# Optimization experiments

Hardware: AMD Instinct MI355X
Metric: run time of the kernel (lower is better)

## Reference

```python
import jax, jax.numpy as jnp
import numpy as np

L = 6
LN_EPS = 1e-5

def _ln(x):
    # LayerNorm over last dim, no affine (matches nn.LayerNorm(D, elementwise_affine=False))
    m = jnp.mean(x, axis=-1, keepdims=True)
    v = jnp.var(x, axis=-1, keepdims=True)
    return (x - m) / jnp.sqrt(v + LN_EPS)

def setup_inputs() -> dict:
    key = jax.random.key(0)
    ks = jax.random.split(key, 6)
    B, S, N, D, V = 2, 2048, 4096, 1024, 32000
    return {
        "input_": jax.random.randint(ks[0], (B, S), 0, V),
        "emb": jax.random.normal(ks[1], (V, D), jnp.float32) * 0.02,
        "Dx": jax.random.normal(ks[2], (D, N), jnp.float32) * 0.02,
        "Dy": jax.random.normal(ks[3], (D, N), jnp.float32) * 0.02,
        "E": jax.random.normal(ks[4], (N, D), jnp.float32) * 0.02,
        "readout": jax.random.normal(ks[5], (D, V), jnp.float32) * 0.02,
    }

def reference(input_, emb, Dx, Dy, E, readout):
    v_ast = emb[input_]  # [B,S,D]
    for _ in range(L):
        x = jax.nn.relu(jnp.einsum('bsd,dn->bsn', v_ast, Dx))  # [B,S,N]
        # linear attention Q@K.mT@V reassociated: x @ (x.mT @ v)
        kv = jnp.einsum('bsn,bsd->bnd', x, v_ast)              # [B,N,D]
        a_ast = jnp.einsum('bsn,bnd->bsd', x, kv)              # [B,S,D]
        y = jax.nn.relu(jnp.einsum('bsd,dn->bsn', a_ast, Dy)) * x  # [B,S,N]
        v_ast = _ln(v_ast + _ln(jnp.einsum('bsn,nd->bsd', y, E)))
    return jnp.einsum('bsd,dv->bsv', v_ast, readout)  # [B,S,vocab]
```

## Files before the change

kernel.cpp:

```cpp
#include <hip/hip_runtime.h>
#include <stdint.h>

typedef unsigned short u16;
typedef __bf16 bf16x8 __attribute__((ext_vector_type(8)));
typedef float  floatx4 __attribute__((ext_vector_type(4)));
typedef u16    ushort4v __attribute__((ext_vector_type(4)));
typedef u16    ushort8v __attribute__((ext_vector_type(8)));

#define B_ 2
#define S_ 2048
#define D_ 1024
#define N_ 4096
#define V_ 32000
#define R_ (B_ * S_)
#define L_ 6

__device__ __forceinline__ u16 f2bf(float f) {
  union { float f; uint32_t u; } v; v.f = f;
  uint32_t r = v.u + 0x7fffu + ((v.u >> 16) & 1u);
  return (u16)(r >> 16);
}
__device__ __forceinline__ float bf2f(u16 h) {
  union { uint32_t u; float f; } v; v.u = ((uint32_t)h) << 16;
  return v.f;
}

__device__ __forceinline__ void gload16(const u16* g, u16* l) {
  auto* gp = (__attribute__((address_space(1))) void*)const_cast<u16*>(g);
  auto* lp = (__attribute__((address_space(3))) void*)l;
  __builtin_amdgcn_global_load_lds(gp, lp, 16, 0, 0);
}

template<int MODE>
__global__ __launch_bounds__(256)
void gemm_bt(const u16* __restrict__ A, const u16* __restrict__ BT,
             void* __restrict__ Cv, const u16* __restrict__ Mul,
             int M, int N, int K, size_t sA, size_t sBT, size_t sC)
{
  __shared__ __align__(16) u16 As[128 * 32];
  __shared__ __align__(16) u16 Bs[128 * 32];

  const int tid  = threadIdx.x;
  const int lane = tid & 63;
  const int wave = tid >> 6;
  const int r = lane & 15;
  const int q = lane >> 4;
  const int wm = (wave >> 1) << 6;
  const int wn = (wave & 1) << 6;

  const int nby = gridDim.y;
  const int bid = blockIdx.y * gridDim.x + blockIdx.x;
  const int bx  = bid / nby;
  const int by  = bid - bx * nby;
  const long m0 = (long)by * 128;
  const long n0 = (long)bx * 128;

  const u16* Ab = A  + (size_t)blockIdx.z * sA;
  const u16* Bb = BT + (size_t)blockIdx.z * sBT;

  const int srow = tid >> 2;
  const int scol = (tid & 3) << 3;
  const u16* a_src0 = Ab + (size_t)(m0 + srow) * K + scol;
  const u16* a_src1 = a_src0 + (size_t)64 * K;
  const u16* b_src0 = Bb + (size_t)(n0 + srow) * K + scol;
  const u16* b_src1 = b_src0 + (size_t)64 * K;
  u16* a_d0 = &As[wave * 512];
  u16* a_d1 = &As[2048 + wave * 512];
  u16* b_d0 = &Bs[wave * 512];
  u16* b_d1 = &Bs[2048 + wave * 512];

  const floatx4 zero = {0.f, 0.f, 0.f, 0.f};
  floatx4 acc[4][4];
#pragma unroll
  for (int i = 0; i < 4; ++i)
#pragma unroll
    for (int j = 0; j < 4; ++j) acc[i][j] = zero;

  for (int kt = 0; kt < K; kt += 32) {
    __syncthreads();
    gload16(a_src0 + kt, a_d0);
    gload16(a_src1 + kt, a_d1);
    gload16(b_src0 + kt, b_d0);
    gload16(b_src1 + kt, b_d1);
    __syncthreads();

    bf16x8 af[4], bfr[4];
#pragma unroll
    for (int i = 0; i < 4; ++i)
      af[i]  = *(const bf16x8*)&As[(wm + i*16 + r) * 32 + (q << 3)];
#pragma unroll
    for (int j = 0; j < 4; ++j)
      bfr[j] = *(const bf16x8*)&Bs[(wn + j*16 + r) * 32 + (q << 3)];
#pragma unroll
    for (int i = 0; i < 4; ++i)
#pragma unroll
      for (int j = 0; j < 4; ++j)
        acc[i][j] = __builtin_amdgcn_mfma_f32_16x16x32_bf16(af[i], bfr[j], acc[i][j], 0, 0, 0);
  }

  const long crow0 = m0 + wm + (q << 2);
  const long ccol0 = n0 + wn + r;
#pragma unroll
  for (int i = 0; i < 4; ++i) {
#pragma unroll
    for (int j = 0; j < 4; ++j) {
      const long col = ccol0 + j * 16;
#pragma unroll
      for (int ii = 0; ii < 4; ++ii) {
        const long row = crow0 + i * 16 + ii;
        float v = acc[i][j][ii];
        if (MODE == 1 || MODE == 2) v = fmaxf(v, 0.f);
        const size_t off = (size_t)row * N + col;
        if (MODE == 2) v *= bf2f(Mul[off]);
        if (MODE == 3) (((float*)Cv) + (size_t)blockIdx.z * sC)[off] = v;
        else           (((u16*)Cv)   + (size_t)blockIdx.z * sC)[off] = f2bf(v);
      }
    }
  }
}

__global__ __launch_bounds__(256)
void transpose_bf16(const u16* __restrict__ src, u16* __restrict__ dst, int R, int C)
{
  __shared__ __align__(16) u16 tile[64][68];
  const int t = threadIdx.x;
  const long r0 = (long)blockIdx.y * 64;
  const long c0 = (long)blockIdx.x * 64;
  const int tc = (t & 15) << 2;
  const int tr = t >> 4;
#pragma unroll
  for (int i = 0; i < 4; ++i) {
    const int rr = tr + (i << 4);
    *(ushort4v*)&tile[rr][tc] = *(const ushort4v*)(src + (size_t)(r0 + rr) * C + c0 + tc);
  }
  __syncthreads();
#pragma unroll
  for (int i = 0; i < 4; ++i) {
    const int cc = tr + (i << 4);
    ushort4v v;
#pragma unroll
    for (int j = 0; j < 4; ++j) v[j] = tile[tc + j][cc];
    *(ushort4v*)(dst + (size_t)(c0 + cc) * R + r0 + tc) = v;
  }
}

__global__ __launch_bounds__(256)
void cvt_transpose(const float* __restrict__ src, u16* __restrict__ dst, int R, int C)
{
  __shared__ __align__(16) u16 tile[64][68];
  const int t = threadIdx.x;
  const long r0 = (long)blockIdx.y * 64;
  const long c0 = (long)blockIdx.x * 64;
  const int tc = (t & 15) << 2;
  const int tr = t >> 4;
#pragma unroll
  for (int i = 0; i < 4; ++i) {
    const int rr = tr + (i << 4);
    const float4 v = *(const float4*)(src + (size_t)(r0 + rr) * C + c0 + tc);
    ushort4v h = {f2bf(v.x), f2bf(v.y), f2bf(v.z), f2bf(v.w)};
    *(ushort4v*)&tile[rr][tc] = h;
  }
  __syncthreads();
#pragma unroll
  for (int i = 0; i < 4; ++i) {
    const int cc = tr + (i << 4);
    ushort4v v;
#pragma unroll
    for (int j = 0; j < 4; ++j) v[j] = tile[tc + j][cc];
    *(ushort4v*)(dst + (size_t)(c0 + cc) * R + r0 + tc) = v;
  }
}

__global__ __launch_bounds__(256)
void embed_k(const int* __restrict__ idx, const float* __restrict__ emb,
             float* __restrict__ vf, u16* __restrict__ vb)
{
  const size_t row = blockIdx.x;
  const int t = threadIdx.x;
  const int id = idx[row];
  const float4 x = ((const float4*)(emb + (size_t)id * D_))[t];
  ((float4*)(vf + row * D_))[t] = x;
  ushort4v h = {f2bf(x.x), f2bf(x.y), f2bf(x.z), f2bf(x.w)};
  ((ushort4v*)(vb + row * D_))[t] = h;
}

__device__ __forceinline__ float block_sum(float v, float* red, int t) {
#pragma unroll
  for (int o = 32; o > 0; o >>= 1) v += __shfl_down(v, o, 64);
  __syncthreads();
  if ((t & 63) == 0) red[t >> 6] = v;
  __syncthreads();
  return red[0] + red[1] + red[2] + red[3];
}

__global__ __launch_bounds__(256)
void ln_k(const float* __restrict__ z, float* __restrict__ vf, u16* __restrict__ vb)
{
  __shared__ float red[4];
  const int t = threadIdx.x;
  const size_t row = blockIdx.x;
  const float4 zv = ((const float4*)(z + row * D_))[t];
  float s = zv.x + zv.y + zv.z + zv.w;
  const float mean = block_sum(s, red, t) * (1.0f / D_);
  float4 d;
  d.x = zv.x - mean; d.y = zv.y - mean; d.z = zv.z - mean; d.w = zv.w - mean;
  float s2 = d.x*d.x + d.y*d.y + d.z*d.z + d.w*d.w;
  const float var = block_sum(s2, red, t) * (1.0f / D_);
  const float inv = rsqrtf(var + 1e-5f);
  const float4 vv = ((const float4*)(vf + row * D_))[t];
  float4 w;
  w.x = vv.x + d.x * inv; w.y = vv.y + d.y * inv;
  w.z = vv.z + d.z * inv; w.w = vv.w + d.w * inv;
  float sw = w.x + w.y + w.z + w.w;
  const float mean2 = block_sum(sw, red, t) * (1.0f / D_);
  float4 d2;
  d2.x = w.x - mean2; d2.y = w.y - mean2; d2.z = w.z - mean2; d2.w = w.w - mean2;
  float s22 = d2.x*d2.x + d2.y*d2.y + d2.z*d2.z + d2.w*d2.w;
  const float var2 = block_sum(s22, red, t) * (1.0f / D_);
  const float inv2 = rsqrtf(var2 + 1e-5f);
  float4 o;
  o.x = d2.x * inv2; o.y = d2.y * inv2; o.z = d2.z * inv2; o.w = d2.w * inv2;
  ((float4*)(vf + row * D_))[t] = o;
  ushort4v h = {f2bf(o.x), f2bf(o.y), f2bf(o.z), f2bf(o.w)};
  ((ushort4v*)(vb + row * D_))[t] = h;
}

extern "C" void kernel_launch(void* const* d_in, const int* in_sizes, int n_in,
                              void* d_out, int out_size, void* d_ws, size_t ws_size,
                              hipStream_t stream)
{
  const int*   inp = (const int*)d_in[0];
  const float* emb = (const float*)d_in[1];
  const float* Dx  = (const float*)d_in[2];
  const float* Dy  = (const float*)d_in[3];
  const float* E   = (const float*)d_in[4];
  const float* ro  = (const float*)d_in[5];
  float* out = (float*)d_out;

  char* p = (char*)d_ws;
  auto take = [&](size_t n) { char* q = p; p += (n + 255) & ~(size_t)255; return q; };
  float* vf  = (float*)take((size_t)R_ * D_ * 4);
  float* zf  = (float*)take((size_t)R_ * D_ * 4);
  u16* vb    = (u16*)take((size_t)R_ * D_ * 2);
  u16* vbT   = (u16*)take((size_t)R_ * D_ * 2);
  u16* xb    = (u16*)take((size_t)R_ * N_ * 2);
  u16* xbT   = (u16*)take((size_t)R_ * N_ * 2);
  u16* yb    = (u16*)take((size_t)R_ * N_ * 2);
  u16* kvT   = (u16*)take((size_t)B_ * D_ * N_ * 2);
  u16* ab    = (u16*)take((size_t)R_ * D_ * 2);
  u16* DxT   = (u16*)take((size_t)D_ * N_ * 2);
  u16* DyT   = (u16*)take((size_t)D_ * N_ * 2);
  u16* ET    = (u16*)take((size_t)D_ * N_ * 2);
  u16* roT   = (u16*)take((size_t)D_ * V_ * 2);

  const dim3 blk(256);

  cvt_transpose<<<dim3(N_/64, D_/64), blk, 0, stream>>>(Dx, DxT, D_, N_);
  cvt_transpose<<<dim3(N_/64, D_/64), blk, 0, stream>>>(Dy, DyT, D_, N_);
  cvt_transpose<<<dim3(D_/64, N_/64), blk, 0, stream>>>(E,  ET,  N_, D_);
  cvt_transpose<<<dim3(V_/64, D_/64), blk, 0, stream>>>(ro, roT, D_, V_);

  embed_k<<<dim3(R_), blk, 0, stream>>>(inp, emb, vf, vb);
  for (int b = 0; b < B_; ++b)
    transpose_bf16<<<dim3(D_/64, S_/64), blk, 0, stream>>>(
        vb + (size_t)b*S_*D_, vbT + (size_t)b*D_*S_, S_, D_);

  for (int l = 0; l < L_; ++l) {
    gemm_bt<1><<<dim3(N_/128, R_/128, 1), blk, 0, stream>>>(
        vb, DxT, xb, nullptr, R_, N_, D_, 0, 0, 0);
    for (int b = 0; b < B_; ++b)
      transpose_bf16<<<dim3(N_/64, S_/64), blk, 0, stream>>>(
          xb + (size_t)b*S_*N_, xbT + (size_t)b*N_*S_, S_, N_);
    gemm_bt<0><<<dim3(N_/128, D_/128, B_), blk, 0, stream>>>(
        vbT, xbT, kvT, nullptr, D_, N_, S_,
        (size_t)D_*S_, (size_t)N_*S_, (size_t)D_*N_);
    gemm_bt<0><<<dim3(D_/128, S_/128, B_), blk, 0, stream>>>(
        xb, kvT, ab, nullptr, S_, D_, N_,
        (size_t)S_*N_, (size_t)D_*N_, (size_t)S_*D_);
    gemm_bt<2><<<dim3(N_/128, R_/128, 1), blk, 0, stream>>>(
        ab, DyT, yb, xb, R_, N_, D_, 0, 0, 0);
    gemm_bt<3><<<dim3(D_/128, R_/128, 1), blk, 0, stream>>>(
        yb, ET, zf, nullptr, R_, D_, N_, 0, 0, 0);
    ln_k<<<dim3(R_), blk, 0, stream>>>(zf, vf, vb);
    for (int b = 0; b < B_; ++b)
      transpose_bf16<<<dim3(D_/64, S_/64), blk, 0, stream>>>(
          vb + (size_t)b*S_*D_, vbT + (size_t)b*D_*S_, S_, D_);
  }

  gemm_bt<3><<<dim3(V_/128, R_/128, 1), blk, 0, stream>>>(
      vb, roT, out, nullptr, R_, V_, D_, 0, 0, 0);
}
```

Baseline: 3.350 ms.

## Add 256x256 double-buffered swizzled GEMM for Dx, Dy and readout projections

Adds a 512-thread GEMM kernel with 256x256 output tiles. It double-buffers LDS through async global_load_lds with explicit vmcnt waits, and XOR-swizzles the LDS layout to avoid bank conflicts on fragment reads. It replaces the 128x128 kernel for the two D->N projections and the vocabulary readout. The same swizzle is also applied to the existing 128x128 kernel. Larger tiles raise operand reuse and hide load latency, at the cost of more registers and 64KB of LDS per block, which may limit occupancy.

```diff
diff --git a/kernel.cpp b/kernel.cpp
--- a/kernel.cpp
+++ b/kernel.cpp
@@ -32,6 +32,121 @@
 }
 
 template<int MODE>
+__global__ __launch_bounds__(512, 2)
+void gemm256(const u16* __restrict__ A, const u16* __restrict__ BT,
+             void* __restrict__ Cv, const u16* __restrict__ Mul,
+             int M, int N, int K, size_t sA, size_t sBT, size_t sC)
+{
+  __shared__ __align__(16) u16 SH[2][2][8192];
+
+  const int tid  = threadIdx.x;
+  const int lane = tid & 63;
+  const int wave = tid >> 6;
+  const int r = lane & 15;
+  const int q = lane >> 4;
+  const int wm = (wave >> 2) << 7;
+  const int wn = (wave & 3) << 6;
+
+  const int nby = gridDim.y;
+  const int bid = blockIdx.y * gridDim.x + blockIdx.x;
+  const int bx  = bid / nby;
+  const int by  = bid - bx * nby;
+  const long m0 = (long)by * 256;
+  const long n0 = (long)bx * 256;
+
+  const u16* Ab = A  + (size_t)blockIdx.z * sA;
+  const u16* Bb = BT + (size_t)blockIdx.z * sBT;
+
+  const int srow = tid >> 2;
+  const int scol = (((tid & 3) ^ ((srow >> 1) & 3)) << 3);
+  const u16* a_s0 = Ab + (size_t)(m0 + srow) * K + scol;
+  const u16* a_s1 = a_s0 + (size_t)128 * K;
+  const u16* b_s0 = Bb + (size_t)(n0 + srow) * K + scol;
+  const u16* b_s1 = b_s0 + (size_t)128 * K;
+  const int dst0 = wave * 512;
+  const int dst1 = 4096 + wave * 512;
+
+  const int cp = (q ^ ((r >> 1) & 3)) << 3;
+  const int abase = (wm + r) * 32 + cp;
+  const int bbase = (wn + r) * 32 + cp;
+
+  const floatx4 zero = {0.f, 0.f, 0.f, 0.f};
+  floatx4 acc[8][4];
+#pragma unroll
+  for (int i = 0; i < 8; ++i)
+#pragma unroll
+    for (int j = 0; j < 4; ++j) acc[i][j] = zero;
+
+  const int nt = K >> 5;
+  gload16(a_s0, &SH[0][0][dst0]);
+  gload16(a_s1, &SH[0][0][dst1]);
+  gload16(b_s0, &SH[0][1][dst0]);
+  gload16(b_s1, &SH[0][1][dst1]);
+
+  int p = 0;
+  for (int t = 0; t < nt; ++t) {
+    const int kt = (t + 1) << 5;
+    if (t + 1 < nt) {
+      gload16(a_s0 + kt, &SH[p ^ 1][0][dst0]);
+      gload16(a_s1 + kt, &SH[p ^ 1][0][dst1]);
+      gload16(b_s0 + kt, &SH[p ^ 1][1][dst0]);
+      gload16(b_s1 + kt, &SH[p ^ 1][1][dst1]);
+      asm volatile("s_waitcnt vmcnt(4)" ::: "memory");
+    } else {
+      asm volatile("s_waitcnt vmcnt(0)" ::: "memory");
+    }
+    __builtin_amdgcn_s_barrier();
+    __builtin_amdgcn_sched_barrier(0);
+    asm volatile("" ::: "memory");
+
+    const u16* As = SH[p][0];
+    const u16* Bs = SH[p][1];
+    bf16x8 bfr[4];
+#pragma unroll
+    for (int j = 0; j < 4; ++j)
+      bfr[j] = *(const bf16x8*)&Bs[bbase + j * 512];
+#pragma unroll
+    for (int h = 0; h < 2; ++h) {
+      bf16x8 af[4];
+#pragma unroll
+      for (int i2 = 0; i2 < 4; ++i2)
+        af[i2] = *(const bf16x8*)&As[abase + (h * 4 + i2) * 512];
+#pragma unroll
+      for (int i2 = 0; i2 < 4; ++i2)
+#pragma unroll
+        for (int j = 0; j < 4; ++j)
+          acc[h * 4 + i2][j] = __builtin_amdgcn_mfma_f32_16x16x32_bf16(
+              af[i2], bfr[j], acc[h * 4 + i2][j], 0, 0, 0);
+    }
+    asm volatile("s_waitcnt lgkmcnt(0)" ::: "memory");
+    __builtin_amdgcn_s_barrier();
+    __builtin_amdgcn_sched_barrier(0);
+    asm volatile("" ::: "memory");
+    p ^= 1;
+  }
+
+  const long crow0 = m0 + wm + (q << 2);
+  const long ccol0 = n0 + wn + r;
+#pragma unroll
+  for (int f = 0; f < 8; ++f) {
+#pragma unroll
+    for (int j = 0; j < 4; ++j) {
+      const long col = ccol0 + j * 16;
+#pragma unroll
+      for (int ii = 0; ii < 4; ++ii) {
+        const long row = crow0 + f * 16 + ii;
+        float v = acc[f][j][ii];
+        if (MODE == 1 || MODE == 2) v = fmaxf(v, 0.f);
+        const size_t off = (size_t)row * N + col;
+        if (MODE == 2) v *= bf2f(Mul[off]);
+        if (MODE == 3) (((float*)Cv) + (size_t)blockIdx.z * sC)[off] = v;
+        else           (((u16*)Cv)   + (size_t)blockIdx.z * sC)[off] = f2bf(v);
+      }
+    }
+  }
+}
+
+template<int MODE>
 __global__ __launch_bounds__(256)
 void gemm_bt(const u16* __restrict__ A, const u16* __restrict__ BT,
              void* __restrict__ Cv, const u16* __restrict__ Mul,
@@ -59,7 +174,7 @@
   const u16* Bb = BT + (size_t)blockIdx.z * sBT;
 
   const int srow = tid >> 2;
-  const int scol = (tid & 3) << 3;
+  const int scol = (((tid & 3) ^ ((srow >> 1) & 3)) << 3);
   const u16* a_src0 = Ab + (size_t)(m0 + srow) * K + scol;
   const u16* a_src1 = a_src0 + (size_t)64 * K;
   const u16* b_src0 = Bb + (size_t)(n0 + srow) * K + scol;
@@ -69,6 +184,8 @@
   u16* b_d0 = &Bs[wave * 512];
   u16* b_d1 = &Bs[2048 + wave * 512];
 
+  const int cp = (q ^ ((r >> 1) & 3)) << 3;
+
   const floatx4 zero = {0.f, 0.f, 0.f, 0.f};
   floatx4 acc[4][4];
 #pragma unroll
@@ -87,10 +204,10 @@
     bf16x8 af[4], bfr[4];
 #pragma unroll
     for (int i = 0; i < 4; ++i)
-      af[i]  = *(const bf16x8*)&As[(wm + i*16 + r) * 32 + (q << 3)];
+      af[i]  = *(const bf16x8*)&As[(wm + i*16 + r) * 32 + cp];
 #pragma unroll
     for (int j = 0; j < 4; ++j)
-      bfr[j] = *(const bf16x8*)&Bs[(wn + j*16 + r) * 32 + (q << 3)];
+      bfr[j] = *(const bf16x8*)&Bs[(wn + j*16 + r) * 32 + cp];
 #pragma unroll
     for (int i = 0; i < 4; ++i)
 #pragma unroll
@@ -254,6 +371,7 @@
   u16* roT   = (u16*)take((size_t)D_ * V_ * 2);
 
   const dim3 blk(256);
+  const dim3 blk512(512);
 
   cvt_transpose<<<dim3(N_/64, D_/64), blk, 0, stream>>>(Dx, DxT, D_, N_);
   cvt_transpose<<<dim3(N_/64, D_/64), blk, 0, stream>>>(Dy, DyT, D_, N_);
@@ -266,7 +384,7 @@
         vb + (size_t)b*S_*D_, vbT + (size_t)b*D_*S_, S_, D_);
 
   for (int l = 0; l < L_; ++l) {
-    gemm_bt<1><<<dim3(N_/128, R_/128, 1), blk, 0, stream>>>(
+    gemm256<1><<<dim3(N_/256, R_/256, 1), blk512, 0, stream>>>(
         vb, DxT, xb, nullptr, R_, N_, D_, 0, 0, 0);
     for (int b = 0; b < B_; ++b)
       transpose_bf16<<<dim3(N_/64, S_/64), blk, 0, stream>>>(
@@ -277,7 +395,7 @@
     gemm_bt<0><<<dim3(D_/128, S_/128, B_), blk, 0, stream>>>(
         xb, kvT, ab, nullptr, S_, D_, N_,
         (size_t)S_*N_, (size_t)D_*N_, (size_t)S_*D_);
-    gemm_bt<2><<<dim3(N_/128, R_/128, 1), blk, 0, stream>>>(
+    gemm256<2><<<dim3(N_/256, R_/256, 1), blk512, 0, stream>>>(
         ab, DyT, yb, xb, R_, N_, D_, 0, 0, 0);
     gemm_bt<3><<<dim3(D_/128, R_/128, 1), blk, 0, stream>>>(
         yb, ET, zf, nullptr, R_, D_, N_, 0, 0, 0);
@@ -287,6 +405,6 @@
           vb + (size_t)b*S_*D_, vbT + (size_t)b*D_*S_, S_, D_);
   }
 
-  gemm_bt<3><<<dim3(V_/128, R_/128, 1), blk, 0, stream>>>(
+  gemm256<3><<<dim3(V_/256, R_/256, 1), blk512, 0, stream>>>(
       vb, roT, out, nullptr, R_, V_, D_, 0, 0, 0);
 }
```

Result: faster. 3.066 ms (-8.5%).
